# Kernel optimization log

Measured on AMD Instinct MI355X. Metric: run time of the kernel, lower is better.

Reference implementation:

```python
import jax, jax.numpy as jnp
import numpy as np

S = 2_000_000   # sequence length (tokens/residues)
P = 1_000_000   # number of 'positive' (pu) indices
E = 20          # number of experts / alphabet size


def setup_inputs() -> dict:
    key = jax.random.key(0)
    k1, k2, k3, k4, k5 = jax.random.split(key, 5)
    # x[0, :, :20] acts as per-token one-hot over the 20-letter alphabet;
    # argmax of uniform noise gives a valid routing index per token.
    x = jax.random.uniform(k1, (1, S, E), dtype=jnp.float32)
    h = jax.random.normal(k2, (S, 2), dtype=jnp.float32)        # 'output1' from inner model
    W = jax.random.normal(k3, (E, 2, 2), dtype=jnp.float32) * 0.5  # per-expert Linear weight [out,in]
    b = jax.random.normal(k4, (E, 2), dtype=jnp.float32) * 0.1     # per-expert Linear bias
    # unique, sorted positive indices (torch.index_select semantics)
    pu_index = jnp.sort(jax.random.permutation(k5, S)[:P]).astype(jnp.int32)
    return {"x": x, "h": h, "W": W, "b": b, "pu_index": pu_index}


def reference(x, h, W, b, pu_index):
    # recognize_res: per-token expert index from one-hot channels 0:20 of x[0]
    res_index = jnp.argmax(x[0, :, :E], axis=-1)                 # [S] int
    # verblizer_function: per-token expert Linear(2,2) + Softmax, fused as
    # gather expert params -> batched matmul -> softmax
    Wt = W[res_index]                                            # [S, 2, 2]
    bt = b[res_index]                                            # [S, 2]
    y = jnp.einsum('si,soi->so', h, Wt) + bt                     # torch Linear: h @ W.T + b
    y = jax.nn.softmax(y, axis=-1)                               # output1 after verblizer
    # pu_train: rows at pu_index first (in pu order), remaining rows after
    n_tok = h.shape[0]
    mask = jnp.zeros((n_tok,), dtype=bool).at[pu_index].set(True)
    non = jnp.nonzero(~mask, size=n_tok - pu_index.shape[0])[0]  # preserves original order
    perm = jnp.concatenate([pu_index.astype(non.dtype), non])
    y2 = y[perm]                                                 # output2
    return (y, y2)
```

## Files before the change

kernel.cpp:

```cpp
#include <hip/hip_runtime.h>
#include <math.h>
#include <limits.h>

#define TPB 256

__global__ __launch_bounds__(TPB) void boundary_kernel(
    const int* __restrict__ pu, int P, int NB, int* __restrict__ boundary)
{
    int i = blockIdx.x * TPB + threadIdx.x;
    if (i >= P) return;
    int cur  = pu[i];
    int lo   = (i == 0) ? 0 : (pu[i - 1] >> 8) + 1;
    int hi   = cur >> 8;
    for (int b = lo; b <= hi; ++b) boundary[b] = i;
    if (i == P - 1)
        for (int b = hi + 1; b <= NB; ++b) boundary[b] = P;
}

__global__ __launch_bounds__(TPB) void verblizer_fused_kernel(
    const float4* __restrict__ x4,
    const float2* __restrict__ h2,
    const float*  __restrict__ W,
    const float*  __restrict__ b,
    const int*    __restrict__ pu,
    const int*    __restrict__ boundary,
    float2*       __restrict__ y,
    float2*       __restrict__ y2,
    int S, int P)
{
    __shared__ float sW[80];
    __shared__ float sb[40];
    __shared__ uint2 pairs[TPB * 5];
    __shared__ int   flags[TPB];
    __shared__ int   wsum[TPB / 64];

    const int t  = threadIdx.x;
    const int bk = blockIdx.x;
    const int B0 = bk * TPB;
    const int nb = min(TPB, S - B0);

    const int r0 = boundary[bk];
    const int r1 = boundary[bk + 1];

    const int pv = (t < r1 - r0) ? pu[r0 + t] : -1;

    const int s_clamped = min(B0 + t, S - 1);
    const float2 hv = h2[s_clamped];

    if (t < 80)       sW[t]      = W[t];
    else if (t < 120) sb[t - 80] = b[t - 80];
    flags[t] = 0;

    const int nchunk = nb * 5;
    const float4* xb = x4 + (size_t)B0 * 5;
#pragma unroll
    for (int j = 0; j < 5; ++j) {
        int m = t + TPB * j;
        if (m < nchunk) {
            float4 v  = xb[m];
            int   tok = m / 5;
            int   c   = m - 5 * tok;
            float best = v.x; int bi = 0;
            if (v.y > best) { best = v.y; bi = 1; }
            if (v.z > best) { best = v.z; bi = 2; }
            if (v.w > best) { best = v.w; bi = 3; }
            pairs[tok * 5 + c] = make_uint2(__float_as_uint(best), (unsigned)(4 * c + bi));
        }
    }
    __syncthreads();

    if (pv >= 0) flags[pv - B0] = 1;
    __syncthreads();

    const bool f   = (t < nb) && flags[t];
    const unsigned long long mask = __ballot(f);
    const int lane = t & 63;
    const int w    = t >> 6;
    if (lane == 0) wsum[w] = __popcll(mask);
    const int cnt = __popcll(mask & ((1ull << lane) - 1ull));
    __syncthreads();

    if (t >= nb) return;

    int base = 0;
#pragma unroll
    for (int ww = 0; ww < TPB / 64; ++ww)
        if (ww < w) base += wsum[ww];
    const int s    = B0 + t;
    const int rank = r0 + base + cnt;

    float best = -INFINITY; int bi = 0;
#pragma unroll
    for (int c = 0; c < 5; ++c) {
        uint2 p = pairs[t * 5 + c];
        float v = __uint_as_float(p.x);
        if (v > best) { best = v; bi = (int)p.y; }
    }

    const float* we = sW + bi * 4;
    float y0 = fmaf(hv.x, we[0], fmaf(hv.y, we[1], sb[bi * 2 + 0]));
    float y1 = fmaf(hv.x, we[2], fmaf(hv.y, we[3], sb[bi * 2 + 1]));
    float mx = fmaxf(y0, y1);
    float e0 = __expf(y0 - mx);
    float e1 = __expf(y1 - mx);
    float inv = 1.0f / (e0 + e1);
    float2 yo = make_float2(e0 * inv, e1 * inv);

    y[s] = yo;
    const int dst = f ? rank : (P + s - rank);
    y2[dst] = yo;
}

extern "C" void kernel_launch(void* const* d_in, const int* in_sizes, int n_in,
                              void* d_out, int out_size, void* d_ws, size_t ws_size,
                              hipStream_t stream) {
    const float* x  = (const float*)d_in[0];
    const float* h  = (const float*)d_in[1];
    const float* W  = (const float*)d_in[2];
    const float* b  = (const float*)d_in[3];
    const int*   pu = (const int*)d_in[4];

    const int S  = in_sizes[1] / 2;
    const int P  = in_sizes[4];
    const int NB = (S + TPB - 1) / TPB;

    int* boundary = (int*)d_ws;

    float2* y  = (float2*)d_out;
    float2* y2 = (float2*)d_out + S;

    boundary_kernel<<<(P + TPB - 1) / TPB, TPB, 0, stream>>>(pu, P, NB, boundary);
    verblizer_fused_kernel<<<NB, TPB, 0, stream>>>(
        (const float4*)x, (const float2*)h, W, b, pu, boundary, y, y2, S, P);
}
```

Before: 255.0 us.

## Process 512-token tiles per block with register-prefetched loads and padded LDS pairs

Each 256-thread block now handles two tokens per thread (a 512-token tile). All ten x float4 loads are issued into registers up front, before any shared-memory work, to raise memory-level parallelism. The per-token argmax pairs are padded to stride 6 so they can be read back as three 16-byte LDS loads. Boundary granularity drops to 128 and the last tile is clamped to S-TILE, which removes bounds checks. The clamp makes the final tile overlap the previous one and rewrite the same outputs, and it assumes S is a multiple of 128 and at least TILE.

```diff
diff --git a/kernel.cpp b/kernel.cpp
--- a/kernel.cpp
+++ b/kernel.cpp
@@ -1,20 +1,21 @@
 #include <hip/hip_runtime.h>
 #include <math.h>
-#include <limits.h>
 
-#define TPB 256
+#define TPB  256
+#define TILE 512
+#define GRAN 128
 
 __global__ __launch_bounds__(TPB) void boundary_kernel(
     const int* __restrict__ pu, int P, int NB, int* __restrict__ boundary)
 {
     int i = blockIdx.x * TPB + threadIdx.x;
     if (i >= P) return;
-    int cur  = pu[i];
-    int lo   = (i == 0) ? 0 : (pu[i - 1] >> 8) + 1;
-    int hi   = cur >> 8;
-    for (int b = lo; b <= hi; ++b) boundary[b] = i;
+    int cur = pu[i];
+    int lo  = (i == 0) ? 0 : (pu[i - 1] / GRAN) + 1;
+    int hi  = cur / GRAN;
+    for (int bb = lo; bb <= hi; ++bb) boundary[bb] = i;
     if (i == P - 1)
-        for (int b = hi + 1; b <= NB; ++b) boundary[b] = P;
+        for (int bb = hi + 1; bb <= NB; ++bb) boundary[bb] = P;
 }
 
 __global__ __launch_bounds__(TPB) void verblizer_fused_kernel(
@@ -28,87 +29,109 @@
     float2*       __restrict__ y2,
     int S, int P)
 {
+    __shared__ __align__(16) uint2 pairs[TILE * 6];
+    __shared__ unsigned char flags[TILE];
+    __shared__ int   wsum[TILE / 64];
     __shared__ float sW[80];
     __shared__ float sb[40];
-    __shared__ uint2 pairs[TPB * 5];
-    __shared__ int   flags[TPB];
-    __shared__ int   wsum[TPB / 64];
 
     const int t  = threadIdx.x;
-    const int bk = blockIdx.x;
-    const int B0 = bk * TPB;
-    const int nb = min(TPB, S - B0);
+    const int B0 = min((int)blockIdx.x * TILE, S - TILE);
 
-    const int r0 = boundary[bk];
-    const int r1 = boundary[bk + 1];
+    const int r0 = boundary[B0 / GRAN];
+    const int r1 = boundary[(B0 + TILE) / GRAN];
+    const int nmark = r1 - r0;
 
-    const int pv = (t < r1 - r0) ? pu[r0 + t] : -1;
-
-    const int s_clamped = min(B0 + t, S - 1);
-    const float2 hv = h2[s_clamped];
+    float4 xv[10];
+    const float4* xb = x4 + (size_t)B0 * 5;
+#pragma unroll
+    for (int j = 0; j < 10; ++j) xv[j] = xb[t + TPB * j];
+    const float2 hA = h2[B0 + t];
+    const float2 hB = h2[B0 + TPB + t];
+    const int pv0 = (t < nmark)       ? pu[r0 + t]       : -1;
+    const int pv1 = (TPB + t < nmark) ? pu[r0 + TPB + t] : -1;
 
     if (t < 80)       sW[t]      = W[t];
     else if (t < 120) sb[t - 80] = b[t - 80];
-    flags[t] = 0;
+    flags[t]       = 0;
+    flags[TPB + t] = 0;
+    pairs[t * 6 + 5]         = make_uint2(0xFF800000u, 0u);
+    pairs[(TPB + t) * 6 + 5] = make_uint2(0xFF800000u, 0u);
 
-    const int nchunk = nb * 5;
-    const float4* xb = x4 + (size_t)B0 * 5;
 #pragma unroll
-    for (int j = 0; j < 5; ++j) {
-        int m = t + TPB * j;
-        if (m < nchunk) {
-            float4 v  = xb[m];
-            int   tok = m / 5;
-            int   c   = m - 5 * tok;
-            float best = v.x; int bi = 0;
-            if (v.y > best) { best = v.y; bi = 1; }
-            if (v.z > best) { best = v.z; bi = 2; }
-            if (v.w > best) { best = v.w; bi = 3; }
-            pairs[tok * 5 + c] = make_uint2(__float_as_uint(best), (unsigned)(4 * c + bi));
-        }
+    for (int j = 0; j < 10; ++j) {
+        int m   = t + TPB * j;
+        int tok = m / 5;
+        int c   = m - 5 * tok;
+        float4 v = xv[j];
+        float best = v.x; int bi = 0;
+        if (v.y > best) { best = v.y; bi = 1; }
+        if (v.z > best) { best = v.z; bi = 2; }
+        if (v.w > best) { best = v.w; bi = 3; }
+        pairs[tok * 6 + c] = make_uint2(__float_as_uint(best), (unsigned)(4 * c + bi));
     }
     __syncthreads();
 
-    if (pv >= 0) flags[pv - B0] = 1;
+    if (pv0 >= 0) flags[pv0 - B0] = 1;
+    if (pv1 >= 0) flags[pv1 - B0] = 1;
     __syncthreads();
 
-    const bool f   = (t < nb) && flags[t];
-    const unsigned long long mask = __ballot(f);
     const int lane = t & 63;
     const int w    = t >> 6;
-    if (lane == 0) wsum[w] = __popcll(mask);
-    const int cnt = __popcll(mask & ((1ull << lane) - 1ull));
+    const bool fA = flags[t] != 0;
+    const bool fB = flags[TPB + t] != 0;
+    const unsigned long long mA = __ballot(fA);
+    const unsigned long long mB = __ballot(fB);
+    if (lane == 0) { wsum[w] = __popcll(mA); wsum[4 + w] = __popcll(mB); }
+    const unsigned long long lmask = (1ull << lane) - 1ull;
+    const int cA = __popcll(mA & lmask);
+    const int cB = __popcll(mB & lmask);
     __syncthreads();
 
-    if (t >= nb) return;
+    int baseA = 0, baseB = 0;
+#pragma unroll
+    for (int ww = 0; ww < 8; ++ww) {
+        int v = wsum[ww];
+        if (ww < w)     baseA += v;
+        if (ww < 4 + w) baseB += v;
+    }
+    const int rankA = r0 + baseA + cA;
+    const int rankB = r0 + baseB + cB;
 
-    int base = 0;
 #pragma unroll
-    for (int ww = 0; ww < TPB / 64; ++ww)
-        if (ww < w) base += wsum[ww];
-    const int s    = B0 + t;
-    const int rank = r0 + base + cnt;
+    for (int half = 0; half < 2; ++half) {
+        const int  tl   = half ? (TPB + t) : t;
+        const float2 hv = half ? hB : hA;
+        const bool f    = half ? fB : fA;
+        const int  rank = half ? rankB : rankA;
 
-    float best = -INFINITY; int bi = 0;
-#pragma unroll
-    for (int c = 0; c < 5; ++c) {
-        uint2 p = pairs[t * 5 + c];
-        float v = __uint_as_float(p.x);
-        if (v > best) { best = v; bi = (int)p.y; }
+        const uint4* pp = (const uint4*)&pairs[tl * 6];
+        uint4 q0 = pp[0], q1 = pp[1], q2 = pp[2];
+        float best = -INFINITY; int bi = 0;
+        {
+            float v;
+            v = __uint_as_float(q0.x); if (v > best) { best = v; bi = (int)q0.y; }
+            v = __uint_as_float(q0.z); if (v > best) { best = v; bi = (int)q0.w; }
+            v = __uint_as_float(q1.x); if (v > best) { best = v; bi = (int)q1.y; }
+            v = __uint_as_float(q1.z); if (v > best) { best = v; bi = (int)q1.w; }
+            v = __uint_as_float(q2.x); if (v > best) { best = v; bi = (int)q2.y; }
+            v = __uint_as_float(q2.z); if (v > best) { best = v; bi = (int)q2.w; }
+        }
+
+        const float* we = sW + bi * 4;
+        float y0 = fmaf(hv.x, we[0], fmaf(hv.y, we[1], sb[bi * 2 + 0]));
+        float y1 = fmaf(hv.x, we[2], fmaf(hv.y, we[3], sb[bi * 2 + 1]));
+        float mx = fmaxf(y0, y1);
+        float e0 = __expf(y0 - mx);
+        float e1 = __expf(y1 - mx);
+        float inv = 1.0f / (e0 + e1);
+        float2 yo = make_float2(e0 * inv, e1 * inv);
+
+        const int s = B0 + tl;
+        y[s] = yo;
+        const int dst = f ? rank : (P + s - rank);
+        y2[dst] = yo;
     }
-
-    const float* we = sW + bi * 4;
-    float y0 = fmaf(hv.x, we[0], fmaf(hv.y, we[1], sb[bi * 2 + 0]));
-    float y1 = fmaf(hv.x, we[2], fmaf(hv.y, we[3], sb[bi * 2 + 1]));
-    float mx = fmaxf(y0, y1);
-    float e0 = __expf(y0 - mx);
-    float e1 = __expf(y1 - mx);
-    float inv = 1.0f / (e0 + e1);
-    float2 yo = make_float2(e0 * inv, e1 * inv);
-
-    y[s] = yo;
-    const int dst = f ? rank : (P + s - rank);
-    y2[dst] = yo;
 }
 
 extern "C" void kernel_launch(void* const* d_in, const int* in_sizes, int n_in,
@@ -122,7 +145,7 @@
 
     const int S  = in_sizes[1] / 2;
     const int P  = in_sizes[4];
-    const int NB = (S + TPB - 1) / TPB;
+    const int NB = S / GRAN;
 
     int* boundary = (int*)d_ws;
 
@@ -130,6 +153,8 @@
     float2* y2 = (float2*)d_out + S;
 
     boundary_kernel<<<(P + TPB - 1) / TPB, TPB, 0, stream>>>(pu, P, NB, boundary);
-    verblizer_fused_kernel<<<NB, TPB, 0, stream>>>(
+
+    const int grid = (S + TILE - 1) / TILE;
+    verblizer_fused_kernel<<<grid, TPB, 0, stream>>>(
         (const float4*)x, (const float2*)h, W, b, pu, boundary, y, y2, S, P);
 }
```

Result: no change. 253.6 us (-0.5%).

## Replace block-level LDS ranking with wave-local shuffle masks, two tokens per thread

Applied to the files above, without the earlier changes.

The fused kernel drops shared memory and all block barriers. Each 64-lane wave now computes its positive-index bitmask with xor-shuffles, which needs the boundary table at 64-token granularity. Each thread handles two tokens, loading all 20 x channels per token straight into registers, so more loads are in flight per thread. Costs: per-lane x reads are strided by 80 bytes and so less coalesced, the last tile is clamped and overlaps the previous one (its duplicate writes are idempotent), and the kernel assumes S is a multiple of 64.

```diff
diff --git a/kernel.cpp b/kernel.cpp
--- a/kernel.cpp
+++ b/kernel.cpp
@@ -1,20 +1,21 @@
 #include <hip/hip_runtime.h>
 #include <math.h>
-#include <limits.h>
 
-#define TPB 256
+#define TPB  256
+#define TILE 512
+#define GRAN 64
 
 __global__ __launch_bounds__(TPB) void boundary_kernel(
     const int* __restrict__ pu, int P, int NB, int* __restrict__ boundary)
 {
     int i = blockIdx.x * TPB + threadIdx.x;
     if (i >= P) return;
-    int cur  = pu[i];
-    int lo   = (i == 0) ? 0 : (pu[i - 1] >> 8) + 1;
-    int hi   = cur >> 8;
-    for (int b = lo; b <= hi; ++b) boundary[b] = i;
+    int cur = pu[i];
+    int lo  = (i == 0) ? 0 : (pu[i - 1] / GRAN) + 1;
+    int hi  = cur / GRAN;
+    for (int bb = lo; bb <= hi; ++bb) boundary[bb] = i;
     if (i == P - 1)
-        for (int b = hi + 1; b <= NB; ++b) boundary[b] = P;
+        for (int bb = hi + 1; bb <= NB; ++bb) boundary[bb] = P;
 }
 
 __global__ __launch_bounds__(TPB) void verblizer_fused_kernel(
@@ -28,87 +29,78 @@
     float2*       __restrict__ y2,
     int S, int P)
 {
-    __shared__ float sW[80];
-    __shared__ float sb[40];
-    __shared__ uint2 pairs[TPB * 5];
-    __shared__ int   flags[TPB];
-    __shared__ int   wsum[TPB / 64];
-
-    const int t  = threadIdx.x;
-    const int bk = blockIdx.x;
-    const int B0 = bk * TPB;
-    const int nb = min(TPB, S - B0);
-
-    const int r0 = boundary[bk];
-    const int r1 = boundary[bk + 1];
-
-    const int pv = (t < r1 - r0) ? pu[r0 + t] : -1;
-
-    const int s_clamped = min(B0 + t, S - 1);
-    const float2 hv = h2[s_clamped];
-
-    if (t < 80)       sW[t]      = W[t];
-    else if (t < 120) sb[t - 80] = b[t - 80];
-    flags[t] = 0;
-
-    const int nchunk = nb * 5;
-    const float4* xb = x4 + (size_t)B0 * 5;
-#pragma unroll
-    for (int j = 0; j < 5; ++j) {
-        int m = t + TPB * j;
-        if (m < nchunk) {
-            float4 v  = xb[m];
-            int   tok = m / 5;
-            int   c   = m - 5 * tok;
-            float best = v.x; int bi = 0;
-            if (v.y > best) { best = v.y; bi = 1; }
-            if (v.z > best) { best = v.z; bi = 2; }
-            if (v.w > best) { best = v.w; bi = 3; }
-            pairs[tok * 5 + c] = make_uint2(__float_as_uint(best), (unsigned)(4 * c + bi));
-        }
-    }
-    __syncthreads();
-
-    if (pv >= 0) flags[pv - B0] = 1;
-    __syncthreads();
-
-    const bool f   = (t < nb) && flags[t];
-    const unsigned long long mask = __ballot(f);
+    const int t    = threadIdx.x;
     const int lane = t & 63;
     const int w    = t >> 6;
-    if (lane == 0) wsum[w] = __popcll(mask);
-    const int cnt = __popcll(mask & ((1ull << lane) - 1ull));
-    __syncthreads();
+    const int B0   = min((int)blockIdx.x * TILE, S - TILE);
 
-    if (t >= nb) return;
+    const int base = B0 + 128 * w;
+    const int s0   = base + lane;
+    const int s1   = base + 64 + lane;
 
-    int base = 0;
+    const int wi  = __builtin_amdgcn_readfirstlane(base >> 6);
+    const int rA0 = boundary[wi];
+    const int rA1 = boundary[wi + 1];
+    const int rB1 = boundary[wi + 2];
+
+    const int pA = pu[min(rA0 + lane, P - 1)];
+    const int pB = pu[min(rA1 + lane, P - 1)];
+
+    float4 xa[5], xbv[5];
+    const float4* xp0 = x4 + (size_t)s0 * 5;
+    const float4* xp1 = x4 + (size_t)s1 * 5;
 #pragma unroll
-    for (int ww = 0; ww < TPB / 64; ++ww)
-        if (ww < w) base += wsum[ww];
-    const int s    = B0 + t;
-    const int rank = r0 + base + cnt;
+    for (int c = 0; c < 5; ++c) { xa[c] = xp0[c]; xbv[c] = xp1[c]; }
+    const float2 h0 = h2[s0];
+    const float2 h1 = h2[s1];
 
-    float best = -INFINITY; int bi = 0;
+    const int nA = rA1 - rA0;
+    const int nB = rB1 - rA1;
+    unsigned long long mA = (lane < nA) ? (1ull << ((unsigned)(pA - base) & 63)) : 0ull;
+    unsigned long long mB = (lane < nB) ? (1ull << ((unsigned)(pB - base - 64) & 63)) : 0ull;
 #pragma unroll
-    for (int c = 0; c < 5; ++c) {
-        uint2 p = pairs[t * 5 + c];
-        float v = __uint_as_float(p.x);
-        if (v > best) { best = v; bi = (int)p.y; }
+    for (int d = 1; d < 64; d <<= 1) {
+        mA |= __shfl_xor(mA, d, 64);
+        mB |= __shfl_xor(mB, d, 64);
     }
+    const unsigned long long lt = (1ull << lane) - 1ull;
+    const int  rankA = rA0 + __popcll(mA & lt);
+    const int  rankB = rA1 + __popcll(mB & lt);
+    const bool fA    = (mA >> lane) & 1;
+    const bool fB    = (mB >> lane) & 1;
 
-    const float* we = sW + bi * 4;
-    float y0 = fmaf(hv.x, we[0], fmaf(hv.y, we[1], sb[bi * 2 + 0]));
-    float y1 = fmaf(hv.x, we[2], fmaf(hv.y, we[3], sb[bi * 2 + 1]));
-    float mx = fmaxf(y0, y1);
-    float e0 = __expf(y0 - mx);
-    float e1 = __expf(y1 - mx);
-    float inv = 1.0f / (e0 + e1);
-    float2 yo = make_float2(e0 * inv, e1 * inv);
+#pragma unroll
+    for (int half = 0; half < 2; ++half) {
+        const float4* xv  = half ? xbv : xa;
+        const float2  hv  = half ? h1 : h0;
+        const int     s   = half ? s1 : s0;
+        const bool    f   = half ? fB : fA;
+        const int     rnk = half ? rankB : rankA;
 
-    y[s] = yo;
-    const int dst = f ? rank : (P + s - rank);
-    y2[dst] = yo;
+        float best = -INFINITY; int bi = 0;
+#pragma unroll
+        for (int c = 0; c < 5; ++c) {
+            float4 v = xv[c];
+            if (v.x > best) { best = v.x; bi = 4 * c + 0; }
+            if (v.y > best) { best = v.y; bi = 4 * c + 1; }
+            if (v.z > best) { best = v.z; bi = 4 * c + 2; }
+            if (v.w > best) { best = v.w; bi = 4 * c + 3; }
+        }
+
+        const float4 wv = *(const float4*)(W + bi * 4);
+        const float2 bv = *(const float2*)(b + bi * 2);
+        float y0 = fmaf(hv.x, wv.x, fmaf(hv.y, wv.y, bv.x));
+        float y1 = fmaf(hv.x, wv.z, fmaf(hv.y, wv.w, bv.y));
+        float mx = fmaxf(y0, y1);
+        float e0 = __expf(y0 - mx);
+        float e1 = __expf(y1 - mx);
+        float inv = 1.0f / (e0 + e1);
+        float2 yo = make_float2(e0 * inv, e1 * inv);
+
+        y[s] = yo;
+        const int dst = f ? rnk : (P + s - rnk);
+        y2[dst] = yo;
+    }
 }
 
 extern "C" void kernel_launch(void* const* d_in, const int* in_sizes, int n_in,
@@ -122,7 +114,7 @@
 
     const int S  = in_sizes[1] / 2;
     const int P  = in_sizes[4];
-    const int NB = (S + TPB - 1) / TPB;
+    const int NB = S / GRAN;
 
     int* boundary = (int*)d_ws;
 
@@ -130,6 +122,8 @@
     float2* y2 = (float2*)d_out + S;
 
     boundary_kernel<<<(P + TPB - 1) / TPB, TPB, 0, stream>>>(pu, P, NB, boundary);
-    verblizer_fused_kernel<<<NB, TPB, 0, stream>>>(
+
+    const int grid = (S + TILE - 1) / TILE;
+    verblizer_fused_kernel<<<grid, TPB, 0, stream>>>(
         (const float4*)x, (const float2*)h, W, b, pu, boundary, y, y2, S, P);
 }
```

Measured after the change: 254.9 us. About the same (-0.0%).
